# Optimization experiments

Hardware: AMD Instinct MI355X
Metric: run time of the kernel (lower is better)

## Reference

```python
import jax, jax.numpy as jnp
import numpy as np
from jax import lax

NPOINT = 1024
NSAMPLE = 32
RADIUS = 0.6
BN_EPS = 1e-5


def square_distance(src, dst):
    # src (B,S,3), dst (B,N,3) -> (B,S,N) squared distances
    d = -2.0 * jnp.einsum('bsc,bnc->bsn', src, dst)
    d = d + jnp.sum(src ** 2, -1)[:, :, None]
    d = d + jnp.sum(dst ** 2, -1)[:, None, :]
    return d


def farthest_point_sample(xyz, npoint):
    B, N, _ = xyz.shape
    bidx = jnp.arange(B)

    def step(carry, _):
        distance, farthest = carry
        centroid = xyz[bidx, farthest]                      # (B,3)
        dist = jnp.sum((xyz - centroid[:, None, :]) ** 2, -1)  # (B,N)
        distance = jnp.minimum(distance, dist)
        new_far = jnp.argmax(distance, -1)
        return (distance, new_far), farthest

    init = (jnp.full((B, N), 1e10, xyz.dtype), jnp.zeros((B,), jnp.int32))
    _, idxs = lax.scan(step, init, None, length=npoint)
    return idxs.T                                            # (B,npoint)


def ball_query(xyz, new_xyz, radius, nsample):
    B, N, _ = xyz.shape
    sqr = square_distance(new_xyz, xyz)                      # (B,S,N)
    idx = jnp.where(sqr <= radius ** 2, jnp.arange(N)[None, None, :], N)
    idx = jnp.sort(idx, axis=-1)[:, :, :nsample]             # (B,S,K)
    first = idx[:, :, :1]
    return jnp.where(idx == N, first, idx)


def gather2(points, idx):
    # points (B,N,C), idx (B,S) -> (B,S,C)
    return jax.vmap(lambda p, i: p[i])(points, idx)


def gather3(points, idx):
    # points (B,N,C), idx (B,S,K) -> (B,S,K,C)
    return jax.vmap(lambda p, i: p[i])(points, idx)


def sa_forward(xyz, features, params):
    fps_idx = lax.stop_gradient(farthest_point_sample(xyz, NPOINT))
    new_xyz = gather2(xyz, fps_idx)                          # (B,S,3)
    idx = lax.stop_gradient(ball_query(xyz, new_xyz, RADIUS, NSAMPLE))
    grouped_xyz = gather3(xyz, idx) - new_xyz[:, :, None, :] # (B,S,K,3)
    grouped_feat = gather3(features.transpose(0, 2, 1), idx) # (B,S,K,C)
    g = jnp.concatenate([grouped_xyz, grouped_feat], -1)     # (B,S,K,C+3)
    g = g.transpose(0, 3, 2, 1)                              # (B,Cin,K,S)
    for w, b, ga, be in params:
        g = jnp.einsum('oc,bcks->boks', w, g) + b[None, :, None, None]
        mu = jnp.mean(g, axis=(0, 2, 3), keepdims=True)
        var = jnp.var(g, axis=(0, 2, 3), keepdims=True)
        g = ga[None, :, None, None] * (g - mu) * lax.rsqrt(var + BN_EPS) \
            + be[None, :, None, None]
        g = jax.nn.relu(g)
    new_features = jnp.max(g, axis=2)                        # (B,Cout,S)
    return new_xyz, new_features


def setup_inputs() -> dict:
    key = jax.random.key(0)
    ks = jax.random.split(key, 8)
    B, N, C = 16, 4096, 128
    cin = C + 3
    mlp = [128, 128, 256]
    inp = {
        'xyz': jax.random.normal(ks[0], (B, N, 3), jnp.float32),
        'features': jax.random.normal(ks[1], (B, C, N), jnp.float32),
    }
    prev = cin
    for i, out in enumerate(mlp):
        inp[f'w{i}'] = jax.random.normal(ks[2 + i], (out, prev), jnp.float32) * 0.05
        inp[f'b{i}'] = jnp.zeros((out,), jnp.float32)
        inp[f'gamma{i}'] = jnp.ones((out,), jnp.float32)
        inp[f'beta{i}'] = jnp.zeros((out,), jnp.float32)
        prev = out
    return inp


def reference(xyz, features, w0, b0, gamma0, beta0, w1, b1, gamma1, beta1,
              w2, b2, gamma2, beta2):
    params = [(w0, b0, gamma0, beta0), (w1, b1, gamma1, beta1),
              (w2, b2, gamma2, beta2)]
    return sa_forward(xyz, features, params)
```

## Files before the change

### kernel.cpp

```cpp
#include <hip/hip_runtime.h>

#define B_ 16
#define N_ 4096
#define S_ 1024
#define K_ 32
#define PITCH2 136
#define PITCH1 168

typedef unsigned long long u64;
typedef short bf16x8 __attribute__((ext_vector_type(8)));
typedef unsigned short u16x8 __attribute__((ext_vector_type(8)));
typedef float f32x4 __attribute__((ext_vector_type(4)));
typedef float f32x2 __attribute__((ext_vector_type(2)));

__device__ __forceinline__ unsigned short f2bf(float f) {
  unsigned u = __float_as_uint(f);
  unsigned r = (u + 0x7FFFu + ((u >> 16) & 1u)) >> 16;
  return (unsigned short)r;
}
__device__ __forceinline__ float bf2f(unsigned short h) {
  return __uint_as_float(((unsigned)h) << 16);
}

#define DPP_MAX(v, ctrl)                                                        \
  {                                                                             \
    int _t = __builtin_amdgcn_update_dpp(__float_as_int(v), __float_as_int(v),  \
                                         ctrl, 0xf, 0xf, false);                \
    v = fmaxf(v, __int_as_float(_t));                                           \
  }

__global__ __launch_bounds__(512) void k_front(
    const float* __restrict__ xyz, float* __restrict__ new_xyz,
    const float* __restrict__ feat, unsigned short* __restrict__ featT,
    const float* __restrict__ w0, const float* __restrict__ w1,
    const float* __restrict__ w2, unsigned short* __restrict__ wbf0,
    unsigned short* __restrict__ wbf1, unsigned short* __restrict__ wbf2,
    float* __restrict__ stats) {
  __shared__ __align__(16) float smem[N_ * 4 + S_ + 64];
  int blk = blockIdx.x, t = threadIdx.x;

  if (blk < 16) {
#pragma clang fp contract(off)
#if __has_builtin(__builtin_amdgcn_s_setprio)
    __builtin_amdgcn_s_setprio(3);
#endif
    float4* pts = (float4*)smem;
    int* idxs = (int*)(smem + N_ * 4);
    u64* km = (u64*)(smem + N_ * 4 + S_);
    int b = blk;
    const float* base = xyz + (size_t)b * N_ * 3;
    for (int i = t; i < N_; i += 512)
      pts[i] = make_float4(base[i * 3], base[i * 3 + 1], base[i * 3 + 2], 0.0f);
    if (t == 0) { idxs[0] = 0; km[0] = 0; km[1] = 0; km[2] = 0; }
    __syncthreads();
    f32x2 px[4], py[4], pz[4], pd[4];
    int i0 = t * 8;
    #pragma unroll
    for (int j = 0; j < 4; ++j) {
      float4 p0 = pts[i0 + 2 * j], p1 = pts[i0 + 2 * j + 1];
      px[j] = (f32x2){p0.x, p1.x};
      py[j] = (f32x2){p0.y, p1.y};
      pz[j] = (f32x2){p0.z, p1.z};
      pd[j] = (f32x2){1e10f, 1e10f};
    }
    int cur = 0;
    int sl = 0;
    for (int it = 0; it < S_; ++it) {
      float4 c = pts[cur];
      f32x2 c2x = (f32x2){c.x, c.x}, c2y = (f32x2){c.y, c.y}, c2z = (f32x2){c.z, c.z};
      float bestv = -1.0f; int besti = 0;
      #pragma unroll
      for (int j = 0; j < 4; ++j) {
        f32x2 dx = px[j] - c2x;
        f32x2 dy = py[j] - c2y;
        f32x2 dz = pz[j] - c2z;
        f32x2 d = (dx * dx + dy * dy) + dz * dz;
        f32x2 dm = __builtin_elementwise_min(pd[j], d);
        pd[j] = dm;
        if (dm.x > bestv) { bestv = dm.x; besti = 2 * j; }
        if (dm.y > bestv) { bestv = dm.y; besti = 2 * j + 1; }
      }
      float v = bestv;
      DPP_MAX(v, 0x111);
      DPP_MAX(v, 0x112);
      DPP_MAX(v, 0x114);
      DPP_MAX(v, 0x118);
      unsigned r0 = (unsigned)__builtin_amdgcn_readlane(__float_as_int(v), 15);
      unsigned r1 = (unsigned)__builtin_amdgcn_readlane(__float_as_int(v), 31);
      unsigned r2 = (unsigned)__builtin_amdgcn_readlane(__float_as_int(v), 47);
      unsigned r3 = (unsigned)__builtin_amdgcn_readlane(__float_as_int(v), 63);
      unsigned ra = r0 > r1 ? r0 : r1;
      unsigned rb = r2 > r3 ? r2 : r3;
      unsigned wmaxb = ra > rb ? ra : rb;
      float wmax = __uint_as_float(wmaxb);
      u64 mask = __ballot(bestv == wmax);
      int owner = __ffsll((long long)mask) - 1;
      int widx = __builtin_amdgcn_readlane(i0 + besti, owner);
      if ((t & 63) == 0)
        atomicMax((unsigned long long*)&km[sl],
                  ((u64)wmaxb << 32) | (unsigned)(4095 - widx));
      __syncthreads();
      u64 k0 = km[sl];
      cur = 4095 - (int)(unsigned)(k0 & 0xFFFFFFFFull);
      if (t == 0) {
        if (it + 1 < S_) idxs[it + 1] = cur;
        km[sl == 0 ? 2 : sl - 1] = 0;
      }
      sl = (sl == 2) ? 0 : sl + 1;
    }
    __syncthreads();
    for (int i = t; i < S_; i += 512) {
      float4 v = pts[idxs[i]];
      size_t o = ((size_t)b * S_ + i) * 3;
      new_xyz[o] = v.x; new_xyz[o + 1] = v.y; new_xyz[o + 2] = v.z;
    }
  } else if (blk < 32) {
    int id = (blk - 16) * 512 + t;
    const int st = 16 * 512;
    for (int i = id; i < 32768; i += st) stats[i] = 0.0f;
    for (int i = id; i < 128 * 160; i += st) {
      int n = i / 160, k = i - n * 160;
      float v = (k < 128) ? w0[n * 131 + 3 + k] : (k < 131) ? w0[n * 131 + k - 128] : 0.0f;
      wbf0[i] = f2bf(v);
    }
    for (int i = id; i < 128 * 128; i += st) wbf1[i] = f2bf(w1[i]);
    for (int i = id; i < 256 * 128; i += st) wbf2[i] = f2bf(w2[i]);
  } else {
    float (*tile)[33] = (float(*)[33])smem;
    int blk2 = blk - 32;
    int n0 = (blk2 & 127) * 32;
    int c0 = ((blk2 >> 7) & 3) * 32;
    int b = blk2 >> 9;
    int tx = t & 31, ty = t >> 5;
    #pragma unroll
    for (int j = 0; j < 32; j += 16)
      tile[ty + j][tx] = feat[((size_t)b * 128 + c0 + ty + j) * N_ + n0 + tx];
    __syncthreads();
    #pragma unroll
    for (int j = 0; j < 32; j += 16)
      featT[((size_t)b * N_ + n0 + ty + j) * 128 + c0 + tx] = f2bf(tile[tx][ty + j]);
  }
}

__global__ __launch_bounds__(256) void k_ballq(const float* __restrict__ xyz,
                                               const float* __restrict__ new_xyz,
                                               int* __restrict__ ball_idx) {
  int b = blockIdx.y;
  int s = blockIdx.x * 4 + (threadIdx.x >> 6);
  int lane = threadIdx.x & 63;
  const float* pb = xyz + (size_t)b * N_ * 3;
  size_t q = (size_t)b * S_ + s;
  float qx = new_xyz[q * 3], qy = new_xyz[q * 3 + 1], qz = new_xyz[q * 3 + 2];
  float sq = __fadd_rn(__fadd_rn(__fmul_rn(qx, qx), __fmul_rn(qy, qy)), __fmul_rn(qz, qz));
  int* out = ball_idx + q * K_;
  int total = 0;
  int first_idx = -1;
  for (int basei = 0; basei < N_; basei += 64) {
    int i = basei + lane;
    float fx = pb[i * 3], fy = pb[i * 3 + 1], fz = pb[i * 3 + 2];
    float dot = __fmul_rn(qx, fx);
    dot = __fadd_rn(dot, __fmul_rn(qy, fy));
    dot = __fadd_rn(dot, __fmul_rn(qz, fz));
    float sd = __fadd_rn(__fadd_rn(__fmul_rn(fx, fx), __fmul_rn(fy, fy)), __fmul_rn(fz, fz));
    float dist = __fadd_rn(__fadd_rn(__fmul_rn(-2.0f, dot), sq), sd);
    bool within = (dist <= 0.36f);
    u64 m = __ballot(within);
    if (first_idx < 0 && m) first_idx = basei + __ffsll((long long)m) - 1;
    if (within) {
      int pos = total + __popcll(m & ((1ull << lane) - 1ull));
      if (pos < K_) out[pos] = i;
    }
    total += (int)__popcll(m);
    if (total >= K_) break;
  }
  if (total < K_) {
    int k2 = total + lane;
    if (k2 < K_) out[k2] = first_idx;
  }
}

#define MFMA(a, b, c) __builtin_amdgcn_mfma_f32_16x16x32_bf16(a, b, c, 0, 0, 0)
#define NTILES 4096

__global__ __launch_bounds__(256) void k_layer1(
    const float* __restrict__ xyz, const float* __restrict__ new_xyz,
    const unsigned short* __restrict__ featT, const int* __restrict__ ball_idx,
    const unsigned short* __restrict__ wbf0, const float* __restrict__ b0,
    unsigned short* __restrict__ y, float* __restrict__ stats) {
  __shared__ __align__(16) unsigned short Wl[128 * PITCH1];
  __shared__ float sbias[128];
  int t = threadIdx.x;
  int w = t >> 6, L = t & 63, lm = L & 15, lg = L >> 4;
  {
    int n = t >> 1, h = t & 1;
    const uint4* wr = (const uint4*)(wbf0 + n * 160 + h * 80);
    uint4* wl = (uint4*)(Wl + n * PITCH1 + h * 80);
    #pragma unroll
    for (int i = 0; i < 10; ++i) wl[i] = wr[i];
    if (t < 128) sbias[t] = b0[t];
  }
  __syncthreads();

  for (int tile = blockIdx.x; tile < NTILES; tile += gridDim.x) {
    int bb = tile >> 8;
    int s0 = (tile & 255) * 4;
    size_t qg = (size_t)bb * S_ + s0 + w;

    int p0 = ball_idx[qg * K_ + lm];
    int p1 = ball_idx[qg * K_ + 16 + lm];
    const unsigned short* f0 = featT + ((size_t)bb * N_ + p0) * 128;
    const unsigned short* f1 = featT + ((size_t)bb * N_ + p1) * 128;
    bf16x8 a0[5], a1[5];
    #pragma unroll
    for (int kt = 0; kt < 4; ++kt) {
      a0[kt] = *(const bf16x8*)(f0 + kt * 32 + lg * 8);
      a1[kt] = *(const bf16x8*)(f1 + kt * 32 + lg * 8);
    }
    a0[4] = (bf16x8){0, 0, 0, 0, 0, 0, 0, 0};
    a1[4] = (bf16x8){0, 0, 0, 0, 0, 0, 0, 0};
    if (lg == 0) {
      float nx = new_xyz[qg * 3], ny = new_xyz[qg * 3 + 1], nz = new_xyz[qg * 3 + 2];
      const float* pp0 = xyz + ((size_t)bb * N_ + p0) * 3;
      const float* pp1 = xyz + ((size_t)bb * N_ + p1) * 3;
      a0[4][0] = (short)f2bf(pp0[0] - nx);
      a0[4][1] = (short)f2bf(pp0[1] - ny);
      a0[4][2] = (short)f2bf(pp0[2] - nz);
      a1[4][0] = (short)f2bf(pp1[0] - nx);
      a1[4][1] = (short)f2bf(pp1[1] - ny);
      a1[4][2] = (short)f2bf(pp1[2] - nz);
    }
    f32x4 acc[2][8];
    #pragma unroll
    for (int mi = 0; mi < 2; ++mi)
      #pragma unroll
      for (int nt = 0; nt < 8; ++nt) acc[mi][nt] = (f32x4){0.f, 0.f, 0.f, 0.f};
    #pragma unroll
    for (int kt = 0; kt < 5; ++kt) {
      int ko = kt * 32 + lg * 8;
      bf16x8 bv[8];
      #pragma unroll
      for (int nt = 0; nt < 8; ++nt)
        bv[nt] = *(const bf16x8*)&Wl[(nt * 16 + lm) * PITCH1 + ko];
      #pragma unroll
      for (int nt = 0; nt < 8; ++nt) {
        acc[0][nt] = MFMA(a0[kt], bv[nt], acc[0][nt]);
        acc[1][nt] = MFMA(a1[kt], bv[nt], acc[1][nt]);
      }
    }
    int slot = tile & 31;
    #pragma unroll
    for (int nt = 0; nt < 8; ++nt) {
      int col = nt * 16 + lm;
      float bo = sbias[col];
      float s1 = 0.f, s2 = 0.f;
      #pragma unroll
      for (int mi = 0; mi < 2; ++mi)
        #pragma unroll
        for (int r = 0; r < 4; ++r) {
          float yv = acc[mi][nt][r] + bo;
          s1 += yv; s2 += yv * yv;
          int ks = mi * 16 + lg * 4 + r;
          y[(qg * K_ + ks) * 128 + col] = f2bf(yv);
        }
      s1 += __shfl_xor(s1, 16); s2 += __shfl_xor(s2, 16);
      s1 += __shfl_xor(s1, 32); s2 += __shfl_xor(s2, 32);
      if (lg == 0) {
        atomicAdd(stats + ((size_t)slot * 128 + col) * 2, s1);
        atomicAdd(stats + ((size_t)slot * 128 + col) * 2 + 1, s2);
      }
    }
  }
}

__global__ __launch_bounds__(256) void k_layer2(
    unsigned short* y, const float* __restrict__ stats,
    const float* __restrict__ gamma, const float* __restrict__ beta,
    const unsigned short* __restrict__ wbf1, const float* __restrict__ b1,
    float* __restrict__ stats2) {
  __shared__ __align__(16) unsigned short Wl[128 * PITCH2];
  __shared__ __align__(16) float sa[128], sd[128];
  __shared__ float sbias[128];
  int t = threadIdx.x;
  int w = t >> 6, L = t & 63, lm = L & 15, lg = L >> 4;
  if (t < 128) {
    float s1 = 0.0f, s2 = 0.0f;
    for (int sl = 0; sl < 32; ++sl) {
      s1 += stats[((size_t)sl * 128 + t) * 2];
      s2 += stats[((size_t)sl * 128 + t) * 2 + 1];
    }
    const float inv = 1.0f / 524288.0f;
    float mu = s1 * inv;
    float var = s2 * inv - mu * mu;
    float a = gamma[t] * rsqrtf(var + 1e-5f);
    sa[t] = a;
    sd[t] = beta[t] - a * mu;
    sbias[t] = b1[t];
  }
  {
    int n = t >> 1, h = t & 1;
    const uint4* wr = (const uint4*)(wbf1 + n * 128 + h * 64);
    uint4* wl = (uint4*)(Wl + n * PITCH2 + h * 64);
    #pragma unroll
    for (int i = 0; i < 8; ++i) wl[i] = wr[i];
  }
  __syncthreads();

  for (int tile = blockIdx.x; tile < NTILES; tile += gridDim.x) {
    int bb = tile >> 8;
    int s0 = (tile & 255) * 4;
    size_t qg = (size_t)bb * S_ + s0 + w;

    const u16x8* yr0 = (const u16x8*)(y + (qg * K_ + lm) * 128);
    const u16x8* yr1 = (const u16x8*)(y + (qg * K_ + 16 + lm) * 128);
    u16x8 raw0[4], raw1[4];
    #pragma unroll
    for (int kt = 0; kt < 4; ++kt) { raw0[kt] = yr0[kt * 4 + lg]; raw1[kt] = yr1[kt * 4 + lg]; }
    bf16x8 a0[4], a1[4];
    #pragma unroll
    for (int kt = 0; kt < 4; ++kt) {
      int c = kt * 32 + lg * 8;
      f32x4 A0 = *(const f32x4*)&sa[c], A1 = *(const f32x4*)&sa[c + 4];
      f32x4 D0 = *(const f32x4*)&sd[c], D1 = *(const f32x4*)&sd[c + 4];
      #pragma unroll
      for (int j = 0; j < 4; ++j) {
        a0[kt][j]     = (short)f2bf(fmaxf(A0[j] * bf2f(raw0[kt][j])     + D0[j], 0.f));
        a0[kt][j + 4] = (short)f2bf(fmaxf(A1[j] * bf2f(raw0[kt][j + 4]) + D1[j], 0.f));
        a1[kt][j]     = (short)f2bf(fmaxf(A0[j] * bf2f(raw1[kt][j])     + D0[j], 0.f));
        a1[kt][j + 4] = (short)f2bf(fmaxf(A1[j] * bf2f(raw1[kt][j + 4]) + D1[j], 0.f));
      }
    }
    f32x4 acc[2][8];
    #pragma unroll
    for (int mi = 0; mi < 2; ++mi)
      #pragma unroll
      for (int nt = 0; nt < 8; ++nt) acc[mi][nt] = (f32x4){0.f, 0.f, 0.f, 0.f};
    #pragma unroll
    for (int kt = 0; kt < 4; ++kt) {
      int ko = kt * 32 + lg * 8;
      bf16x8 bv[8];
      #pragma unroll
      for (int nt = 0; nt < 8; ++nt)
        bv[nt] = *(const bf16x8*)&Wl[(nt * 16 + lm) * PITCH2 + ko];
      #pragma unroll
      for (int nt = 0; nt < 8; ++nt) {
        acc[0][nt] = MFMA(a0[kt], bv[nt], acc[0][nt]);
        acc[1][nt] = MFMA(a1[kt], bv[nt], acc[1][nt]);
      }
    }
    int slot = tile & 31;
    #pragma unroll
    for (int nt = 0; nt < 8; ++nt) {
      int col = nt * 16 + lm;
      float bo = sbias[col];
      float s1 = 0.f, s2 = 0.f;
      #pragma unroll
      for (int mi = 0; mi < 2; ++mi)
        #pragma unroll
        for (int r = 0; r < 4; ++r) {
          float yv = acc[mi][nt][r] + bo;
          s1 += yv; s2 += yv * yv;
          int ks = mi * 16 + lg * 4 + r;
          y[(qg * K_ + ks) * 128 + col] = f2bf(yv);
        }
      s1 += __shfl_xor(s1, 16); s2 += __shfl_xor(s2, 16);
      s1 += __shfl_xor(s1, 32); s2 += __shfl_xor(s2, 32);
      if (lg == 0) {
        atomicAdd(stats2 + ((size_t)slot * 128 + col) * 2, s1);
        atomicAdd(stats2 + ((size_t)slot * 128 + col) * 2 + 1, s2);
      }
    }
  }
}

__global__ __launch_bounds__(256) void k_layer3(
    const unsigned short* __restrict__ y, const float* __restrict__ stats2,
    const float* __restrict__ gamma, const float* __restrict__ beta,
    const unsigned short* __restrict__ wbf2, const float* __restrict__ b2,
    unsigned short* __restrict__ ymax, unsigned short* __restrict__ ymin,
    float* __restrict__ stats3) {
  __shared__ __align__(16) unsigned short Wl[256 * PITCH2];
  __shared__ __align__(16) float sa[128], sd[128];
  __shared__ float sbias[256];
  int t = threadIdx.x;
  int w = t >> 6, L = t & 63, lm = L & 15, lg = L >> 4;
  if (t < 128) {
    float s1 = 0.0f, s2 = 0.0f;
    for (int sl = 0; sl < 32; ++sl) {
      s1 += stats2[((size_t)sl * 128 + t) * 2];
      s2 += stats2[((size_t)sl * 128 + t) * 2 + 1];
    }
    const float inv = 1.0f / 524288.0f;
    float mu = s1 * inv;
    float var = s2 * inv - mu * mu;
    float a = gamma[t] * rsqrtf(var + 1e-5f);
    sa[t] = a;
    sd[t] = beta[t] - a * mu;
  }
  sbias[t] = b2[t];
  {
    const uint4* wr = (const uint4*)(wbf2 + (size_t)t * 128);
    uint4* wl = (uint4*)(Wl + t * PITCH2);
    #pragma unroll
    for (int i = 0; i < 16; ++i) wl[i] = wr[i];
  }
  __syncthreads();

  for (int tile = blockIdx.x; tile < NTILES; tile += gridDim.x) {
    int bb = tile >> 8;
    int s0 = (tile & 255) * 4;
    size_t qg = (size_t)bb * S_ + s0 + w;

    const u16x8* yr0 = (const u16x8*)(y + (qg * K_ + lm) * 128);
    const u16x8* yr1 = (const u16x8*)(y + (qg * K_ + 16 + lm) * 128);
    u16x8 raw0[4], raw1[4];
    #pragma unroll
    for (int kt = 0; kt < 4; ++kt) { raw0[kt] = yr0[kt * 4 + lg]; raw1[kt] = yr1[kt * 4 + lg]; }
    bf16x8 a0[4], a1[4];
    #pragma unroll
    for (int kt = 0; kt < 4; ++kt) {
      int c = kt * 32 + lg * 8;
      f32x4 A0 = *(const f32x4*)&sa[c], A1 = *(const f32x4*)&sa[c + 4];
      f32x4 D0 = *(const f32x4*)&sd[c], D1 = *(const f32x4*)&sd[c + 4];
      #pragma unroll
      for (int j = 0; j < 4; ++j) {
        a0[kt][j]     = (short)f2bf(fmaxf(A0[j] * bf2f(raw0[kt][j])     + D0[j], 0.f));
        a0[kt][j + 4] = (short)f2bf(fmaxf(A1[j] * bf2f(raw0[kt][j + 4]) + D1[j], 0.f));
        a1[kt][j]     = (short)f2bf(fmaxf(A0[j] * bf2f(raw1[kt][j])     + D0[j], 0.f));
        a1[kt][j + 4] = (short)f2bf(fmaxf(A1[j] * bf2f(raw1[kt][j + 4]) + D1[j], 0.f));
      }
    }
    int slot = tile & 31;
    #pragma unroll
    for (int h = 0; h < 2; ++h) {
      f32x4 acc[2][8];
      #pragma unroll
      for (int mi = 0; mi < 2; ++mi)
        #pragma unroll
        for (int nt = 0; nt < 8; ++nt) acc[mi][nt] = (f32x4){0.f, 0.f, 0.f, 0.f};
      #pragma unroll
      for (int kt = 0; kt < 4; ++kt) {
        int ko = kt * 32 + lg * 8;
        bf16x8 bv[8];
        #pragma unroll
        for (int nt = 0; nt < 8; ++nt)
          bv[nt] = *(const bf16x8*)&Wl[(h * 128 + nt * 16 + lm) * PITCH2 + ko];
        #pragma unroll
        for (int nt = 0; nt < 8; ++nt) {
          acc[0][nt] = MFMA(a0[kt], bv[nt], acc[0][nt]);
          acc[1][nt] = MFMA(a1[kt], bv[nt], acc[1][nt]);
        }
      }
      #pragma unroll
      for (int nt = 0; nt < 8; ++nt) {
        int col = nt * 16 + lm;
        int o = h * 128 + col;
        float bo = sbias[o];
        float s1 = 0.f, s2 = 0.f, mx = -3.4e38f, mn = 3.4e38f;
        #pragma unroll
        for (int mi = 0; mi < 2; ++mi)
          #pragma unroll
          for (int r = 0; r < 4; ++r) {
            float yv = acc[mi][nt][r] + bo;
            s1 += yv; s2 += yv * yv;
            mx = fmaxf(mx, yv); mn = fminf(mn, yv);
          }
        s1 += __shfl_xor(s1, 16); s2 += __shfl_xor(s2, 16);
        s1 += __shfl_xor(s1, 32); s2 += __shfl_xor(s2, 32);
        mx = fmaxf(mx, __shfl_xor(mx, 16)); mx = fmaxf(mx, __shfl_xor(mx, 32));
        mn = fminf(mn, __shfl_xor(mn, 16)); mn = fminf(mn, __shfl_xor(mn, 32));
        if (lg == 0) {
          ymax[qg * 256 + o] = f2bf(mx);
          ymin[qg * 256 + o] = f2bf(mn);
          atomicAdd(stats3 + ((size_t)slot * 256 + o) * 2, s1);
          atomicAdd(stats3 + ((size_t)slot * 256 + o) * 2 + 1, s2);
        }
      }
    }
  }
}

__global__ __launch_bounds__(256) void k_final(const unsigned short* __restrict__ ymax,
                                               const unsigned short* __restrict__ ymin,
                                               const float* __restrict__ stats3,
                                               const float* __restrict__ gamma,
                                               const float* __restrict__ beta,
                                               float* __restrict__ out2) {
  __shared__ float tile[32][33];
  __shared__ float smA[32], smD[32];
  int b = blockIdx.z, o0 = blockIdx.y * 32, s0 = blockIdx.x * 32;
  int tx = threadIdx.x, ty = threadIdx.y;
  if (ty == 0) {
    int c = o0 + tx;
    float s1 = 0.0f, s2 = 0.0f;
    for (int sl = 0; sl < 32; ++sl) {
      s1 += stats3[((size_t)sl * 256 + c) * 2];
      s2 += stats3[((size_t)sl * 256 + c) * 2 + 1];
    }
    const float inv = 1.0f / 524288.0f;
    float mu = s1 * inv;
    float var = s2 * inv - mu * mu;
    float a = gamma[c] * rsqrtf(var + 1e-5f);
    smA[tx] = a;
    smD[tx] = beta[c] - a * mu;
  }
  __syncthreads();
  float a_rd = smA[tx];
  #pragma unroll
  for (int j = 0; j < 32; j += 8) {
    size_t src = ((size_t)b * S_ + s0 + ty + j) * 256 + o0 + tx;
    tile[ty + j][tx] = (a_rd >= 0.0f) ? bf2f(ymax[src]) : bf2f(ymin[src]);
  }
  __syncthreads();
  #pragma unroll
  for (int j = 0; j < 32; j += 8) {
    float a = smA[ty + j], dd = smD[ty + j];
    out2[((size_t)b * 256 + o0 + ty + j) * S_ + s0 + tx] = fmaxf(a * tile[tx][ty + j] + dd, 0.0f);
  }
}

extern "C" void kernel_launch(void* const* d_in, const int* in_sizes, int n_in,
                              void* d_out, int out_size, void* d_ws, size_t ws_size,
                              hipStream_t stream) {
  (void)in_sizes; (void)n_in; (void)out_size; (void)ws_size;
  const float* xyz  = (const float*)d_in[0];
  const float* feat = (const float*)d_in[1];
  const float* w0   = (const float*)d_in[2];
  const float* b0   = (const float*)d_in[3];
  const float* ga0  = (const float*)d_in[4];
  const float* be0  = (const float*)d_in[5];
  const float* w1   = (const float*)d_in[6];
  const float* b1   = (const float*)d_in[7];
  const float* ga1  = (const float*)d_in[8];
  const float* be1  = (const float*)d_in[9];
  const float* w2   = (const float*)d_in[10];
  const float* b2   = (const float*)d_in[11];
  const float* ga2  = (const float*)d_in[12];
  const float* be2  = (const float*)d_in[13];

  float* out_xyz  = (float*)d_out;
  float* out_feat = out_xyz + (size_t)B_ * S_ * 3;

  char* ws = (char*)d_ws;
  size_t off = 0;
  auto alloc = [&](size_t bytes) -> void* {
    void* p = ws + off;
    off += (bytes + 255) & ~(size_t)255;
    return p;
  };
  unsigned short* featT = (unsigned short*)alloc((size_t)B_ * N_ * 128 * 2);
  int*   ball  = (int*)alloc((size_t)B_ * S_ * K_ * 4);
  float* stats = (float*)alloc(32768 * 4);
  unsigned short* wbf0 = (unsigned short*)alloc(128 * 160 * 2);
  unsigned short* wbf1 = (unsigned short*)alloc(128 * 128 * 2);
  unsigned short* wbf2 = (unsigned short*)alloc(256 * 128 * 2);
  unsigned short* ymaxb = (unsigned short*)alloc((size_t)B_ * S_ * 256 * 2);
  unsigned short* yminb = (unsigned short*)alloc((size_t)B_ * S_ * 256 * 2);
  unsigned short* y = (unsigned short*)alloc((size_t)B_ * S_ * K_ * 128 * 2);

  k_front<<<16 + 16 + 8192, 512, 0, stream>>>(xyz, out_xyz, feat, featT,
                                              w0, w1, w2, wbf0, wbf1, wbf2, stats);
  k_ballq<<<dim3(256, 16), 256, 0, stream>>>(xyz, out_xyz, ball);
  k_layer1<<<768, 256, 0, stream>>>(xyz, out_xyz, featT, ball, wbf0, b0, y, stats);
  k_layer2<<<1024, 256, 0, stream>>>(y, stats, ga0, be0, wbf1, b1, stats + 8192);
  k_layer3<<<512, 256, 0, stream>>>(y, stats + 8192, ga1, be1, wbf2, b2,
                                    ymaxb, yminb, stats + 16384);
  k_final<<<dim3(32, 8, 16), dim3(32, 8), 0, stream>>>(ymaxb, yminb, stats + 16384,
                                                       ga2, be2, out_feat);
}
```

Before: 978.9 us.

## Overlap FPS with fused ball-query and layer-1 via persistent blocks and flags

Farthest point sampling blocks now publish progress through per-batch global flags every 16 centroids. A persistent grid of 240 worker blocks does the weight conversion and feature transpose, then runs a fused ball-query plus layer-1 MFMA stage as soon as the needed centroids exist. The separate ball-query kernel and the ball-index buffer are removed. The goal is to hide the serial FPS latency behind the gather and GEMM work. The design relies on all 256 blocks being co-resident, since workers spin-wait on flags, and ball queries now run on only 240 blocks.

Result: faster. 950.6 us (-2.9%).

```diff
diff --git a/kernel.cpp b/kernel.cpp
--- a/kernel.cpp
+++ b/kernel.cpp
@@ -29,14 +29,24 @@
     v = fmaxf(v, __int_as_float(_t));                                           \
   }
 
+#define MFMA(a, b, c) __builtin_amdgcn_mfma_f32_16x16x32_bf16(a, b, c, 0, 0, 0)
+
+__global__ __launch_bounds__(256) void k_init(float* __restrict__ stats,
+                                              unsigned* __restrict__ sync) {
+  int id = blockIdx.x * 256 + threadIdx.x;
+  for (int i = id; i < 32768; i += 8192) stats[i] = 0.0f;
+  if (id < 32) sync[id] = 0u;
+}
+
 __global__ __launch_bounds__(512) void k_front(
     const float* __restrict__ xyz, float* __restrict__ new_xyz,
     const float* __restrict__ feat, unsigned short* __restrict__ featT,
     const float* __restrict__ w0, const float* __restrict__ w1,
     const float* __restrict__ w2, unsigned short* __restrict__ wbf0,
     unsigned short* __restrict__ wbf1, unsigned short* __restrict__ wbf2,
-    float* __restrict__ stats) {
-  __shared__ __align__(16) float smem[N_ * 4 + S_ + 64];
+    const float* __restrict__ b0, unsigned short* __restrict__ y,
+    float* __restrict__ stats, unsigned* __restrict__ sync) {
+  __shared__ __align__(16) float smem[N_ * 4 + 16];
   int blk = blockIdx.x, t = threadIdx.x;
 
   if (blk < 16) {
@@ -45,13 +55,12 @@
     __builtin_amdgcn_s_setprio(3);
 #endif
     float4* pts = (float4*)smem;
-    int* idxs = (int*)(smem + N_ * 4);
-    u64* km = (u64*)(smem + N_ * 4 + S_);
+    u64* km = (u64*)(smem + N_ * 4);
     int b = blk;
     const float* base = xyz + (size_t)b * N_ * 3;
     for (int i = t; i < N_; i += 512)
       pts[i] = make_float4(base[i * 3], base[i * 3 + 1], base[i * 3 + 2], 0.0f);
-    if (t == 0) { idxs[0] = 0; km[0] = 0; km[1] = 0; km[2] = 0; }
+    if (t == 0) { km[0] = 0; km[1] = 0; km[2] = 0; }
     __syncthreads();
     f32x2 px[4], py[4], pz[4], pd[4];
     int i0 = t * 8;
@@ -67,6 +76,10 @@
     int sl = 0;
     for (int it = 0; it < S_; ++it) {
       float4 c = pts[cur];
+      if (t == 0) {
+        size_t o = ((size_t)b * S_ + it) * 3;
+        new_xyz[o] = c.x; new_xyz[o + 1] = c.y; new_xyz[o + 2] = c.z;
+      }
       f32x2 c2x = (f32x2){c.x, c.x}, c2y = (f32x2){c.y, c.y}, c2z = (f32x2){c.z, c.z};
       float bestv = -1.0f; int besti = 0;
       #pragma unroll
@@ -102,171 +115,167 @@
       __syncthreads();
       u64 k0 = km[sl];
       cur = 4095 - (int)(unsigned)(k0 & 0xFFFFFFFFull);
+      if (t == 64) km[sl == 0 ? 2 : sl - 1] = 0;
+      if (t == 0 && (it & 15) == 15) {
+        __threadfence();
+        __hip_atomic_store(sync + b, (unsigned)(it + 1), __ATOMIC_RELEASE,
+                           __HIP_MEMORY_SCOPE_AGENT);
+      }
+      sl = (sl == 2) ? 0 : sl + 1;
+    }
+  } else {
+    int wid = blk - 16;
+    {
+      int id = wid * 512 + t;
+      const int st = 240 * 512;
+      for (int i = id; i < 128 * 160; i += st) {
+        int n = i / 160, k = i - n * 160;
+        float v = (k < 128) ? w0[n * 131 + 3 + k] : (k < 131) ? w0[n * 131 + k - 128] : 0.0f;
+        wbf0[i] = f2bf(v);
+      }
+      for (int i = id; i < 128 * 128; i += st) wbf1[i] = f2bf(w1[i]);
+      for (int i = id; i < 256 * 128; i += st) wbf2[i] = f2bf(w2[i]);
+    }
+    {
+      float (*tile)[33] = (float(*)[33])smem;
+      int tx = t & 31, ty = t >> 5;
+      for (int tt = wid; tt < 8192; tt += 240) {
+        int n0 = (tt & 127) * 32;
+        int c0 = ((tt >> 7) & 3) * 32;
+        int bb = tt >> 9;
+        __syncthreads();
+        #pragma unroll
+        for (int j = 0; j < 32; j += 16)
+          tile[ty + j][tx] = feat[((size_t)bb * 128 + c0 + ty + j) * N_ + n0 + tx];
+        __syncthreads();
+        #pragma unroll
+        for (int j = 0; j < 32; j += 16)
+          featT[((size_t)bb * N_ + n0 + ty + j) * 128 + c0 + tx] = f2bf(tile[tx][ty + j]);
+      }
+    }
+    __threadfence();
+    __syncthreads();
+    if (t == 0) {
+      __hip_atomic_fetch_add(sync + 16, 1u, __ATOMIC_RELEASE, __HIP_MEMORY_SCOPE_AGENT);
+      while (__hip_atomic_load(sync + 16, __ATOMIC_ACQUIRE, __HIP_MEMORY_SCOPE_AGENT) < 240u)
+        __builtin_amdgcn_s_sleep(16);
+    }
+    __syncthreads();
+    unsigned short* Wl = (unsigned short*)smem;
+    float* sbias = smem + 10752;
+    int* ballsc = (int*)(smem + 10752 + 128);
+    {
+      int n = t >> 2, h = t & 3;
+      const uint4* wr = (const uint4*)(wbf0 + n * 160 + h * 40);
+      uint4* wl = (uint4*)(Wl + n * PITCH1 + h * 40);
+      #pragma unroll
+      for (int i = 0; i < 5; ++i) wl[i] = wr[i];
+      if (t < 128) sbias[t] = b0[t];
+    }
+    __syncthreads();
+
+    int wv = t >> 6, lane = t & 63;
+    int lm = lane & 15, lg = lane >> 4;
+    for (int grp = wid; grp < 2048; grp += 240) {
+      int bb = grp & 15, g = grp >> 4;
+      int qb = g * 8;
       if (t == 0) {
-        if (it + 1 < S_) idxs[it + 1] = cur;
-        km[sl == 0 ? 2 : sl - 1] = 0;
-      }
-      sl = (sl == 2) ? 0 : sl + 1;
-    }
-    __syncthreads();
-    for (int i = t; i < S_; i += 512) {
-      float4 v = pts[idxs[i]];
-      size_t o = ((size_t)b * S_ + i) * 3;
-      new_xyz[o] = v.x; new_xyz[o + 1] = v.y; new_xyz[o + 2] = v.z;
-    }
-  } else if (blk < 32) {
-    int id = (blk - 16) * 512 + t;
-    const int st = 16 * 512;
-    for (int i = id; i < 32768; i += st) stats[i] = 0.0f;
-    for (int i = id; i < 128 * 160; i += st) {
-      int n = i / 160, k = i - n * 160;
-      float v = (k < 128) ? w0[n * 131 + 3 + k] : (k < 131) ? w0[n * 131 + k - 128] : 0.0f;
-      wbf0[i] = f2bf(v);
-    }
-    for (int i = id; i < 128 * 128; i += st) wbf1[i] = f2bf(w1[i]);
-    for (int i = id; i < 256 * 128; i += st) wbf2[i] = f2bf(w2[i]);
-  } else {
-    float (*tile)[33] = (float(*)[33])smem;
-    int blk2 = blk - 32;
-    int n0 = (blk2 & 127) * 32;
-    int c0 = ((blk2 >> 7) & 3) * 32;
-    int b = blk2 >> 9;
-    int tx = t & 31, ty = t >> 5;
-    #pragma unroll
-    for (int j = 0; j < 32; j += 16)
-      tile[ty + j][tx] = feat[((size_t)b * 128 + c0 + ty + j) * N_ + n0 + tx];
-    __syncthreads();
-    #pragma unroll
-    for (int j = 0; j < 32; j += 16)
-      featT[((size_t)b * N_ + n0 + ty + j) * 128 + c0 + tx] = f2bf(tile[tx][ty + j]);
-  }
-}
-
-__global__ __launch_bounds__(256) void k_ballq(const float* __restrict__ xyz,
-                                               const float* __restrict__ new_xyz,
-                                               int* __restrict__ ball_idx) {
-  int b = blockIdx.y;
-  int s = blockIdx.x * 4 + (threadIdx.x >> 6);
-  int lane = threadIdx.x & 63;
-  const float* pb = xyz + (size_t)b * N_ * 3;
-  size_t q = (size_t)b * S_ + s;
-  float qx = new_xyz[q * 3], qy = new_xyz[q * 3 + 1], qz = new_xyz[q * 3 + 2];
-  float sq = __fadd_rn(__fadd_rn(__fmul_rn(qx, qx), __fmul_rn(qy, qy)), __fmul_rn(qz, qz));
-  int* out = ball_idx + q * K_;
-  int total = 0;
-  int first_idx = -1;
-  for (int basei = 0; basei < N_; basei += 64) {
-    int i = basei + lane;
-    float fx = pb[i * 3], fy = pb[i * 3 + 1], fz = pb[i * 3 + 2];
-    float dot = __fmul_rn(qx, fx);
-    dot = __fadd_rn(dot, __fmul_rn(qy, fy));
-    dot = __fadd_rn(dot, __fmul_rn(qz, fz));
-    float sd = __fadd_rn(__fadd_rn(__fmul_rn(fx, fx), __fmul_rn(fy, fy)), __fmul_rn(fz, fz));
-    float dist = __fadd_rn(__fadd_rn(__fmul_rn(-2.0f, dot), sq), sd);
-    bool within = (dist <= 0.36f);
-    u64 m = __ballot(within);
-    if (first_idx < 0 && m) first_idx = basei + __ffsll((long long)m) - 1;
-    if (within) {
-      int pos = total + __popcll(m & ((1ull << lane) - 1ull));
-      if (pos < K_) out[pos] = i;
-    }
-    total += (int)__popcll(m);
-    if (total >= K_) break;
-  }
-  if (total < K_) {
-    int k2 = total + lane;
-    if (k2 < K_) out[k2] = first_idx;
-  }
-}
-
-#define MFMA(a, b, c) __builtin_amdgcn_mfma_f32_16x16x32_bf16(a, b, c, 0, 0, 0)
-#define NTILES 4096
-
-__global__ __launch_bounds__(256) void k_layer1(
-    const float* __restrict__ xyz, const float* __restrict__ new_xyz,
-    const unsigned short* __restrict__ featT, const int* __restrict__ ball_idx,
-    const unsigned short* __restrict__ wbf0, const float* __restrict__ b0,
-    unsigned short* __restrict__ y, float* __restrict__ stats) {
-  __shared__ __align__(16) unsigned short Wl[128 * PITCH1];
-  __shared__ float sbias[128];
-  int t = threadIdx.x;
-  int w = t >> 6, L = t & 63, lm = L & 15, lg = L >> 4;
-  {
-    int n = t >> 1, h = t & 1;
-    const uint4* wr = (const uint4*)(wbf0 + n * 160 + h * 80);
-    uint4* wl = (uint4*)(Wl + n * PITCH1 + h * 80);
-    #pragma unroll
-    for (int i = 0; i < 10; ++i) wl[i] = wr[i];
-    if (t < 128) sbias[t] = b0[t];
-  }
-  __syncthreads();
-
-  for (int tile = blockIdx.x; tile < NTILES; tile += gridDim.x) {
-    int bb = tile >> 8;
-    int s0 = (tile & 255) * 4;
-    size_t qg = (size_t)bb * S_ + s0 + w;
-
-    int p0 = ball_idx[qg * K_ + lm];
-    int p1 = ball_idx[qg * K_ + 16 + lm];
-    const unsigned short* f0 = featT + ((size_t)bb * N_ + p0) * 128;
-    const unsigned short* f1 = featT + ((size_t)bb * N_ + p1) * 128;
-    bf16x8 a0[5], a1[5];
-    #pragma unroll
-    for (int kt = 0; kt < 4; ++kt) {
-      a0[kt] = *(const bf16x8*)(f0 + kt * 32 + lg * 8);
-      a1[kt] = *(const bf16x8*)(f1 + kt * 32 + lg * 8);
-    }
-    a0[4] = (bf16x8){0, 0, 0, 0, 0, 0, 0, 0};
-    a1[4] = (bf16x8){0, 0, 0, 0, 0, 0, 0, 0};
-    if (lg == 0) {
-      float nx = new_xyz[qg * 3], ny = new_xyz[qg * 3 + 1], nz = new_xyz[qg * 3 + 2];
-      const float* pp0 = xyz + ((size_t)bb * N_ + p0) * 3;
-      const float* pp1 = xyz + ((size_t)bb * N_ + p1) * 3;
-      a0[4][0] = (short)f2bf(pp0[0] - nx);
-      a0[4][1] = (short)f2bf(pp0[1] - ny);
-      a0[4][2] = (short)f2bf(pp0[2] - nz);
-      a1[4][0] = (short)f2bf(pp1[0] - nx);
-      a1[4][1] = (short)f2bf(pp1[1] - ny);
-      a1[4][2] = (short)f2bf(pp1[2] - nz);
-    }
-    f32x4 acc[2][8];
-    #pragma unroll
-    for (int mi = 0; mi < 2; ++mi)
-      #pragma unroll
-      for (int nt = 0; nt < 8; ++nt) acc[mi][nt] = (f32x4){0.f, 0.f, 0.f, 0.f};
-    #pragma unroll
-    for (int kt = 0; kt < 5; ++kt) {
-      int ko = kt * 32 + lg * 8;
-      bf16x8 bv[8];
-      #pragma unroll
-      for (int nt = 0; nt < 8; ++nt)
-        bv[nt] = *(const bf16x8*)&Wl[(nt * 16 + lm) * PITCH1 + ko];
+        while (__hip_atomic_load(sync + bb, __ATOMIC_ACQUIRE,
+                                 __HIP_MEMORY_SCOPE_AGENT) < (unsigned)(qb + 8))
+          __builtin_amdgcn_s_sleep(16);
+      }
+      __syncthreads();
+      int s = qb + wv;
+      size_t q = (size_t)bb * S_ + s;
+      const float* pb = xyz + (size_t)bb * N_ * 3;
+      float qx = new_xyz[q * 3], qy = new_xyz[q * 3 + 1], qz = new_xyz[q * 3 + 2];
+      float sq = __fadd_rn(__fadd_rn(__fmul_rn(qx, qx), __fmul_rn(qy, qy)), __fmul_rn(qz, qz));
+      int* out = ballsc + wv * 32;
+      int total = 0;
+      int first_idx = -1;
+      for (int basei = 0; basei < N_; basei += 64) {
+        int i = basei + lane;
+        float fx = pb[i * 3], fy = pb[i * 3 + 1], fz = pb[i * 3 + 2];
+        float dot = __fmul_rn(qx, fx);
+        dot = __fadd_rn(dot, __fmul_rn(qy, fy));
+        dot = __fadd_rn(dot, __fmul_rn(qz, fz));
+        float sd = __fadd_rn(__fadd_rn(__fmul_rn(fx, fx), __fmul_rn(fy, fy)), __fmul_rn(fz, fz));
+        float dist = __fadd_rn(__fadd_rn(__fmul_rn(-2.0f, dot), sq), sd);
+        bool within = (dist <= 0.36f);
+        u64 m = __ballot(within);
+        if (first_idx < 0 && m) first_idx = basei + __ffsll((long long)m) - 1;
+        if (within) {
+          int pos = total + __popcll(m & ((1ull << lane) - 1ull));
+          if (pos < K_) out[pos] = i;
+        }
+        total += (int)__popcll(m);
+        if (total >= K_) break;
+      }
+      if (total < K_) {
+        int k2 = total + lane;
+        if (k2 < K_) out[k2] = first_idx;
+      }
+      int p0 = out[lm];
+      int p1 = out[16 + lm];
+      const unsigned short* f0 = featT + ((size_t)bb * N_ + p0) * 128;
+      const unsigned short* f1 = featT + ((size_t)bb * N_ + p1) * 128;
+      bf16x8 a0[5], a1[5];
+      #pragma unroll
+      for (int kt = 0; kt < 4; ++kt) {
+        a0[kt] = *(const bf16x8*)(f0 + kt * 32 + lg * 8);
+        a1[kt] = *(const bf16x8*)(f1 + kt * 32 + lg * 8);
+      }
+      a0[4] = (bf16x8){0, 0, 0, 0, 0, 0, 0, 0};
+      a1[4] = (bf16x8){0, 0, 0, 0, 0, 0, 0, 0};
+      if (lg == 0) {
+        const float* pp0 = xyz + ((size_t)bb * N_ + p0) * 3;
+        const float* pp1 = xyz + ((size_t)bb * N_ + p1) * 3;
+        a0[4][0] = (short)f2bf(pp0[0] - qx);
+        a0[4][1] = (short)f2bf(pp0[1] - qy);
+        a0[4][2] = (short)f2bf(pp0[2] - qz);
+        a1[4][0] = (short)f2bf(pp1[0] - qx);
+        a1[4][1] = (short)f2bf(pp1[1] - qy);
+        a1[4][2] = (short)f2bf(pp1[2] - qz);
+      }
+      f32x4 acc[2][8];
+      #pragma unroll
+      for (int mi = 0; mi < 2; ++mi)
+        #pragma unroll
+        for (int nt = 0; nt < 8; ++nt) acc[mi][nt] = (f32x4){0.f, 0.f, 0.f, 0.f};
+      #pragma unroll
+      for (int kt = 0; kt < 5; ++kt) {
+        int ko = kt * 32 + lg * 8;
+        bf16x8 bv[8];
+        #pragma unroll
+        for (int nt = 0; nt < 8; ++nt)
+          bv[nt] = *(const bf16x8*)&Wl[(nt * 16 + lm) * PITCH1 + ko];
+        #pragma unroll
+        for (int nt = 0; nt < 8; ++nt) {
+          acc[0][nt] = MFMA(a0[kt], bv[nt], acc[0][nt]);
+          acc[1][nt] = MFMA(a1[kt], bv[nt], acc[1][nt]);
+        }
+      }
+      int slot = (bb * 256 + g * 2 + (wv >> 2)) & 31;
       #pragma unroll
       for (int nt = 0; nt < 8; ++nt) {
-        acc[0][nt] = MFMA(a0[kt], bv[nt], acc[0][nt]);
-        acc[1][nt] = MFMA(a1[kt], bv[nt], acc[1][nt]);
-      }
-    }
-    int slot = tile & 31;
-    #pragma unroll
-    for (int nt = 0; nt < 8; ++nt) {
-      int col = nt * 16 + lm;
-      float bo = sbias[col];
-      float s1 = 0.f, s2 = 0.f;
-      #pragma unroll
-      for (int mi = 0; mi < 2; ++mi)
-        #pragma unroll
-        for (int r = 0; r < 4; ++r) {
-          float yv = acc[mi][nt][r] + bo;
-          s1 += yv; s2 += yv * yv;
-          int ks = mi * 16 + lg * 4 + r;
-          y[(qg * K_ + ks) * 128 + col] = f2bf(yv);
+        int col = nt * 16 + lm;
+        float bo = sbias[col];
+        float s1 = 0.f, s2 = 0.f;
+        #pragma unroll
+        for (int mi = 0; mi < 2; ++mi)
+          #pragma unroll
+          for (int r = 0; r < 4; ++r) {
+            float yv = acc[mi][nt][r] + bo;
+            s1 += yv; s2 += yv * yv;
+            int ks = mi * 16 + lg * 4 + r;
+            y[(q * K_ + ks) * 128 + col] = f2bf(yv);
+          }
+        s1 += __shfl_xor(s1, 16); s2 += __shfl_xor(s2, 16);
+        s1 += __shfl_xor(s1, 32); s2 += __shfl_xor(s2, 32);
+        if (lg == 0) {
+          atomicAdd(stats + ((size_t)slot * 128 + col) * 2, s1);
+          atomicAdd(stats + ((size_t)slot * 128 + col) * 2 + 1, s2);
         }
-      s1 += __shfl_xor(s1, 16); s2 += __shfl_xor(s2, 16);
-      s1 += __shfl_xor(s1, 32); s2 += __shfl_xor(s2, 32);
-      if (lg == 0) {
-        atomicAdd(stats + ((size_t)slot * 128 + col) * 2, s1);
-        atomicAdd(stats + ((size_t)slot * 128 + col) * 2 + 1, s2);
       }
     }
   }
@@ -305,7 +314,7 @@
   }
   __syncthreads();
 
-  for (int tile = blockIdx.x; tile < NTILES; tile += gridDim.x) {
+  for (int tile = blockIdx.x; tile < 4096; tile += gridDim.x) {
     int bb = tile >> 8;
     int s0 = (tile & 255) * 4;
     size_t qg = (size_t)bb * S_ + s0 + w;
@@ -405,7 +414,7 @@
   }
   __syncthreads();
 
-  for (int tile = blockIdx.x; tile < NTILES; tile += gridDim.x) {
+  for (int tile = blockIdx.x; tile < 4096; tile += gridDim.x) {
     int bb = tile >> 8;
     int s0 = (tile & 255) * 4;
     size_t qg = (size_t)bb * S_ + s0 + w;
@@ -548,7 +557,6 @@
     return p;
   };
   unsigned short* featT = (unsigned short*)alloc((size_t)B_ * N_ * 128 * 2);
-  int*   ball  = (int*)alloc((size_t)B_ * S_ * K_ * 4);
   float* stats = (float*)alloc(32768 * 4);
   unsigned short* wbf0 = (unsigned short*)alloc(128 * 160 * 2);
   unsigned short* wbf1 = (unsigned short*)alloc(128 * 128 * 2);
@@ -556,11 +564,11 @@
   unsigned short* ymaxb = (unsigned short*)alloc((size_t)B_ * S_ * 256 * 2);
   unsigned short* yminb = (unsigned short*)alloc((size_t)B_ * S_ * 256 * 2);
   unsigned short* y = (unsigned short*)alloc((size_t)B_ * S_ * K_ * 128 * 2);
-
-  k_front<<<16 + 16 + 8192, 512, 0, stream>>>(xyz, out_xyz, feat, featT,
-                                              w0, w1, w2, wbf0, wbf1, wbf2, stats);
-  k_ballq<<<dim3(256, 16), 256, 0, stream>>>(xyz, out_xyz, ball);
-  k_layer1<<<768, 256, 0, stream>>>(xyz, out_xyz, featT, ball, wbf0, b0, y, stats);
+  unsigned* sync = (unsigned*)alloc(128);
+
+  k_init<<<32, 256, 0, stream>>>(stats, sync);
+  k_front<<<256, 512, 0, stream>>>(xyz, out_xyz, feat, featT, w0, w1, w2,
+                                   wbf0, wbf1, wbf2, b0, y, stats, sync);
   k_layer2<<<1024, 256, 0, stream>>>(y, stats, ga0, be0, wbf1, b1, stats + 8192);
   k_layer3<<<512, 256, 0, stream>>>(y, stats + 8192, ga1, be1, wbf2, b2,
                                     ymaxb, yminb, stats + 16384);
```
